# Kernel tuning notes

Hardware: AMD Instinct MI355X
Metric: run time of the kernel (lower is better)

## Reference

```python
import jax, jax.numpy as jnp
import numpy as np

N_EMBD = 384
BLOCK_SIZE = 256

def setup_inputs() -> dict:
    key = jax.random.key(0)
    k1, k2 = jax.random.split(key)
    B, T = 512, 256
    x = jax.random.normal(k1, (B, T, N_EMBD), dtype=jnp.float32)
    # nn.Linear(384, 192, bias=False): store as [in, out] so projection is x @ w
    w_qkv = jax.random.normal(k2, (N_EMBD, 3 * 64), dtype=jnp.float32) * (1.0 / np.sqrt(N_EMBD))
    return {"x": x, "w_qkv": w_qkv}

def reference(x, w_qkv):
    B, T, C = x.shape  # C == n_embd == 384
    qkv = jnp.einsum('btc,cd->btd', x, w_qkv)       # [B,T,3*hs]
    q, k, v = jnp.split(qkv, 3, axis=-1)            # each [B,T,hs]
    scale = 1.0 / jnp.sqrt(jnp.float32(C))          # NOTE: scales by full embed dim C, per source
    wei = jnp.einsum('btd,bsd->bts', q, k) * scale  # [B,T,T]
    causal = jnp.tril(jnp.ones((T, T), dtype=bool))
    wei = jnp.where(causal, wei, -jnp.inf)
    wei = jax.nn.softmax(wei, axis=-1)
    # dropout is identity in eval mode
    return jnp.einsum('bts,bsd->btd', wei, v)       # [B,T,hs]
```

## Files before the change

### kernel.cpp

```cpp
#include <hip/hip_runtime.h>
#include <hip/hip_bf16.h>


constexpr int B  = 512;
constexpr int T  = 256;
constexpr int C  = 384;
constexpr int HS = 64;
constexpr long BT = (long)B * T;
constexpr long PLANE = BT * HS;
constexpr float SCALE = 0.05103103630798288f;

constexpr int NT   = 192;
constexpr int MT   = 128;
constexpr int BK   = 64;
constexpr int ROWP = 72;
constexpr int VP   = 264;

typedef _Float16 f16x8 __attribute__((ext_vector_type(8)));
typedef _Float16 f16x4 __attribute__((ext_vector_type(4)));
typedef __fp16   fp16x2_raw __attribute__((ext_vector_type(2)));
typedef float    f32x4 __attribute__((ext_vector_type(4)));

__global__ __launch_bounds__(256)
void wt_kernel(const float* __restrict__ w, _Float16* __restrict__ wt) {
    const int idx = blockIdx.x * 256 + threadIdx.x;
    if (idx < NT * C) {
        const int n = idx / C, k = idx % C;
        wt[idx] = (_Float16)w[k * NT + n];
    }
}

__global__ __launch_bounds__(256)
void proj_kernel(const float* __restrict__ x, const _Float16* __restrict__ wt,
                 _Float16* __restrict__ qp, _Float16* __restrict__ kp,
                 _Float16* __restrict__ vtp) {
    __shared__ __align__(16) _Float16 XL[MT * ROWP];
    __shared__ __align__(16) _Float16 WL[NT * ROWP];

    const int tid  = threadIdx.x;
    const int lane = tid & 63;
    const int wv   = tid >> 6;
    const int wm   = wv >> 1, wn = wv & 1;
    const int l15  = lane & 15, quad = lane >> 4;
    const long row0 = (long)blockIdx.x * MT;

    f32x4 acc[4][6];
#pragma unroll
    for (int mi = 0; mi < 4; ++mi)
#pragma unroll
        for (int ni = 0; ni < 6; ++ni) acc[mi][ni] = (f32x4)0.f;

    for (int kc = 0; kc < C / BK; ++kc) {
        const int k0 = kc * BK;
        __syncthreads();
#pragma unroll
        for (int i = 0; i < 8; ++i) {
            const int flat = tid + 256 * i;
            const int r = flat >> 4, seg = flat & 15;
            const float4 xv = *(const float4*)(x + (row0 + r) * C + k0 + seg * 4);
            union { fp16x2_raw h[2]; uint2 u; } cvt;
            cvt.h[0] = __builtin_amdgcn_cvt_pkrtz(xv.x, xv.y);
            cvt.h[1] = __builtin_amdgcn_cvt_pkrtz(xv.z, xv.w);
            *(uint2*)&XL[r * ROWP + seg * 4] = cvt.u;
        }
#pragma unroll
        for (int i = 0; i < 6; ++i) {
            const int flat = tid + 256 * i;
            const int n = flat >> 3, seg = flat & 7;
            *(uint4*)&WL[n * ROWP + seg * 8] = *(const uint4*)(wt + n * C + k0 + seg * 8);
        }
        __syncthreads();

#pragma unroll
        for (int s = 0; s < 2; ++s) {
            const int kk = s * 32 + quad * 8;
            f16x8 a[4], bfr[6];
#pragma unroll
            for (int mi = 0; mi < 4; ++mi)
                a[mi] = *(const f16x8*)&XL[(wm * 64 + mi * 16 + l15) * ROWP + kk];
#pragma unroll
            for (int ni = 0; ni < 6; ++ni)
                bfr[ni] = *(const f16x8*)&WL[(wn * 96 + ni * 16 + l15) * ROWP + kk];
#pragma unroll
            for (int mi = 0; mi < 4; ++mi)
#pragma unroll
                for (int ni = 0; ni < 6; ++ni)
                    acc[mi][ni] = __builtin_amdgcn_mfma_f32_16x16x32_f16(
                        a[mi], bfr[ni], acc[mi][ni], 0, 0, 0);
        }
    }

#pragma unroll
    for (int mi = 0; mi < 4; ++mi) {
        const long grow0 = row0 + wm * 64 + mi * 16 + quad * 4;
        const int bb = (int)(grow0 >> 8);
        const int t0 = (int)(grow0 & 255);
#pragma unroll
        for (int ni = 0; ni < 6; ++ni) {
            const int colbase = wn * 96 + ni * 16;
            const int col = colbase + l15;
            if (colbase < 64) {
#pragma unroll
                for (int r = 0; r < 4; ++r)
                    qp[(grow0 + r) * HS + col] = (_Float16)acc[mi][ni][r];
            } else if (colbase < 128) {
#pragma unroll
                for (int r = 0; r < 4; ++r)
                    kp[(grow0 + r) * HS + (col - 64)] = (_Float16)acc[mi][ni][r];
            } else {
                f16x4 pv;
#pragma unroll
                for (int r = 0; r < 4; ++r) pv[r] = (_Float16)acc[mi][ni][r];
                *(f16x4*)&vtp[(long)bb * (HS * T) + (col - 128) * T + t0] = pv;
            }
        }
    }
}

__global__ __launch_bounds__(256)
void attn_kernel(const _Float16* __restrict__ qp, const _Float16* __restrict__ kp,
                 const _Float16* __restrict__ vtp, float* __restrict__ out) {
    __shared__ __align__(16) _Float16 VL[HS * VP];

    const int b = blockIdx.x, tid = threadIdx.x;
    const int lane = tid & 63, w = tid >> 6;
    const int l15 = lane & 15, quad = lane >> 4;

    const _Float16* Vg = vtp + (long)b * (HS * T);
#pragma unroll
    for (int i = 0; i < 8; ++i) {
        const int flat = tid + 256 * i;
        const int r = flat >> 5, seg = flat & 31;
        *(uint4*)&VL[r * VP + seg * 8] = *(const uint4*)(Vg + r * T + seg * 8);
    }
    __syncthreads();

    const _Float16* Qg = qp + ((long)b * T + w * 64) * HS;
    const _Float16* Kg = kp + (long)b * T * HS;
    f16x8 qf[4][2];
#pragma unroll
    for (int ni = 0; ni < 4; ++ni)
#pragma unroll
        for (int ks = 0; ks < 2; ++ks)
            qf[ni][ks] = *(const f16x8*)(Qg + (ni * 16 + l15) * HS + ks * 32 + quad * 8);

    f32x4 o[4][4];
#pragma unroll
    for (int di = 0; di < 4; ++di)
#pragma unroll
        for (int ni = 0; ni < 4; ++ni) o[di][ni] = (f32x4)0.f;
    float lp[4] = {0.f, 0.f, 0.f, 0.f};

    for (int c = 0; c <= w; ++c) {
        const bool diag = (c == w);
#pragma unroll
        for (int kt = 0; kt < 4; ++kt) {
            const int key0 = c * 64 + kt * 16;
            const f16x8 ka0 = *(const f16x8*)(Kg + (key0 + l15) * HS + quad * 8);
            const f16x8 ka1 = *(const f16x8*)(Kg + (key0 + l15) * HS + 32 + quad * 8);
            f16x4 va[4];
#pragma unroll
            for (int di = 0; di < 4; ++di)
                va[di] = *(const f16x4*)&VL[(di * 16 + l15) * VP + key0 + quad * 4];
#pragma unroll
            for (int ni = 0; ni < 4; ++ni) {
                if (diag && kt > ni) continue;
                f32x4 s = {0.f, 0.f, 0.f, 0.f};
                s = __builtin_amdgcn_mfma_f32_16x16x32_f16(ka0, qf[ni][0], s, 0, 0, 0);
                s = __builtin_amdgcn_mfma_f32_16x16x32_f16(ka1, qf[ni][1], s, 0, 0, 0);
                const bool dmask = diag && (kt == ni);
                f16x4 pb;
                float psum = 0.f;
#pragma unroll
                for (int r = 0; r < 4; ++r) {
                    float pr = __expf(s[r] * SCALE);
                    pr = (dmask && (quad * 4 + r > l15)) ? 0.f : pr;
                    psum += pr;
                    pb[r] = (_Float16)pr;
                }
                lp[ni] += psum;
#pragma unroll
                for (int di = 0; di < 4; ++di)
                    o[di][ni] = __builtin_amdgcn_mfma_f32_16x16x16f16(
                        va[di], pb, o[di][ni], 0, 0, 0);
            }
        }
    }

#pragma unroll
    for (int ni = 0; ni < 4; ++ni) {
        float v = lp[ni];
        v += __shfl_xor(v, 16, 64);
        v += __shfl_xor(v, 32, 64);
        lp[ni] = 1.0f / v;
    }

    float* ob = out + ((long)b * T + w * 64) * HS;
#pragma unroll
    for (int ni = 0; ni < 4; ++ni)
#pragma unroll
        for (int di = 0; di < 4; ++di) {
            float4 val;
            val.x = o[di][ni][0] * lp[ni];
            val.y = o[di][ni][1] * lp[ni];
            val.z = o[di][ni][2] * lp[ni];
            val.w = o[di][ni][3] * lp[ni];
            *(float4*)&ob[(ni * 16 + l15) * HS + di * 16 + quad * 4] = val;
        }
}

extern "C" void kernel_launch(void* const* d_in, const int* in_sizes, int n_in,
                              void* d_out, int out_size, void* d_ws, size_t ws_size,
                              hipStream_t stream) {
    const float* x = (const float*)d_in[0];
    const float* w = (const float*)d_in[1];
    float* out = (float*)d_out;

    _Float16* qp  = (_Float16*)d_ws;
    _Float16* kp  = qp + PLANE;
    _Float16* vtp = kp + PLANE;
    _Float16* wt  = vtp + PLANE;

    wt_kernel<<<dim3((NT * C + 255) / 256), dim3(256), 0, stream>>>(w, wt);
    proj_kernel<<<dim3((unsigned)(BT / MT)), dim3(256), 0, stream>>>(x, wt, qp, kp, vtp);
    attn_kernel<<<dim3(B), dim3(256), 0, stream>>>(qp, kp, vtp, out);
}
```

Before: 322.9 us.

## Fuse QKV projection and causal attention into one per-batch kernel

```diff
diff --git a/kernel.cpp b/kernel.cpp
--- a/kernel.cpp
+++ b/kernel.cpp
@@ -1,20 +1,17 @@
 #include <hip/hip_runtime.h>
-#include <hip/hip_bf16.h>
 
 
 constexpr int B  = 512;
 constexpr int T  = 256;
 constexpr int C  = 384;
 constexpr int HS = 64;
-constexpr long BT = (long)B * T;
-constexpr long PLANE = BT * HS;
-constexpr float SCALE = 0.05103103630798288f;
-
-constexpr int NT   = 192;
-constexpr int MT   = 128;
-constexpr int BK   = 64;
+constexpr int NT = 192;
+constexpr int BK = 64;
+constexpr int NKC = C / BK;
 constexpr int ROWP = 72;
 constexpr int VP   = 264;
+constexpr float SCALE = 0.05103103630798288f;
+constexpr float QSC   = SCALE * 1.4426950408889634f;
 
 typedef _Float16 f16x8 __attribute__((ext_vector_type(8)));
 typedef _Float16 f16x4 __attribute__((ext_vector_type(4)));
@@ -30,19 +27,20 @@
     }
 }
 
-__global__ __launch_bounds__(256)
-void proj_kernel(const float* __restrict__ x, const _Float16* __restrict__ wt,
-                 _Float16* __restrict__ qp, _Float16* __restrict__ kp,
-                 _Float16* __restrict__ vtp) {
-    __shared__ __align__(16) _Float16 XL[MT * ROWP];
-    __shared__ __align__(16) _Float16 WL[NT * ROWP];
+__global__ __launch_bounds__(512)
+void fused_kernel(const float* __restrict__ x, const _Float16* __restrict__ wt,
+                  float* __restrict__ out) {
+    __shared__ __align__(16) _Float16 XL[T * ROWP];
+    __shared__ __align__(16) _Float16 WL[NT * BK];
+    __shared__ __align__(16) _Float16 QL[T * HS];
+    __shared__ __align__(16) _Float16 KL[T * HS];
+    __shared__ __align__(16) _Float16 VTL[HS * VP];
 
     const int tid  = threadIdx.x;
-    const int lane = tid & 63;
-    const int wv   = tid >> 6;
+    const int lane = tid & 63, wv = tid >> 6;
+    const int l15  = lane & 15, quad = lane >> 4;
     const int wm   = wv >> 1, wn = wv & 1;
-    const int l15  = lane & 15, quad = lane >> 4;
-    const long row0 = (long)blockIdx.x * MT;
+    const float* xb = x + (long)blockIdx.x * T * C;
 
     f32x4 acc[4][6];
 #pragma unroll
@@ -50,163 +48,155 @@
 #pragma unroll
         for (int ni = 0; ni < 6; ++ni) acc[mi][ni] = (f32x4)0.f;
 
-    for (int kc = 0; kc < C / BK; ++kc) {
-        const int k0 = kc * BK;
+    float4 xv[8];
+    uint4  wvr[3];
+#pragma unroll
+    for (int i = 0; i < 8; ++i) {
+        const int flat = tid + 512 * i, r = flat >> 4, seg = flat & 15;
+        xv[i] = *(const float4*)(xb + r * C + seg * 4);
+    }
+#pragma unroll
+    for (int i = 0; i < 3; ++i) {
+        const int u = tid + 512 * i, n = u >> 3, sl = u & 7;
+        wvr[i] = *(const uint4*)(wt + n * C + sl * 8);
+    }
+
+    for (int kc = 0; kc < NKC; ++kc) {
         __syncthreads();
 #pragma unroll
         for (int i = 0; i < 8; ++i) {
-            const int flat = tid + 256 * i;
-            const int r = flat >> 4, seg = flat & 15;
-            const float4 xv = *(const float4*)(x + (row0 + r) * C + k0 + seg * 4);
-            union { fp16x2_raw h[2]; uint2 u; } cvt;
-            cvt.h[0] = __builtin_amdgcn_cvt_pkrtz(xv.x, xv.y);
-            cvt.h[1] = __builtin_amdgcn_cvt_pkrtz(xv.z, xv.w);
-            *(uint2*)&XL[r * ROWP + seg * 4] = cvt.u;
-        }
-#pragma unroll
-        for (int i = 0; i < 6; ++i) {
-            const int flat = tid + 256 * i;
-            const int n = flat >> 3, seg = flat & 7;
-            *(uint4*)&WL[n * ROWP + seg * 8] = *(const uint4*)(wt + n * C + k0 + seg * 8);
+            const int flat = tid + 512 * i, r = flat >> 4, seg = flat & 15;
+            union { fp16x2_raw h[2]; uint2 u; } cv;
+            cv.h[0] = __builtin_amdgcn_cvt_pkrtz(xv[i].x, xv[i].y);
+            cv.h[1] = __builtin_amdgcn_cvt_pkrtz(xv[i].z, xv[i].w);
+            *(uint2*)&XL[r * ROWP + seg * 4] = cv.u;
+        }
+#pragma unroll
+        for (int i = 0; i < 3; ++i) {
+            const int u = tid + 512 * i, n = u >> 3, sl = u & 7;
+            *(uint4*)&WL[n * BK + ((sl ^ (n & 7)) << 3)] = wvr[i];
         }
         __syncthreads();
-
+        if (kc + 1 < NKC) {
+            const int k0 = (kc + 1) * BK;
+#pragma unroll
+            for (int i = 0; i < 8; ++i) {
+                const int flat = tid + 512 * i, r = flat >> 4, seg = flat & 15;
+                xv[i] = *(const float4*)(xb + r * C + k0 + seg * 4);
+            }
+#pragma unroll
+            for (int i = 0; i < 3; ++i) {
+                const int u = tid + 512 * i, n = u >> 3, sl = u & 7;
+                wvr[i] = *(const uint4*)(wt + n * C + k0 + sl * 8);
+            }
+        }
 #pragma unroll
         for (int s = 0; s < 2; ++s) {
             const int kk = s * 32 + quad * 8;
-            f16x8 a[4], bfr[6];
+            const int slot = kk >> 3;
+            f16x8 a[4], bf[6];
 #pragma unroll
             for (int mi = 0; mi < 4; ++mi)
                 a[mi] = *(const f16x8*)&XL[(wm * 64 + mi * 16 + l15) * ROWP + kk];
 #pragma unroll
-            for (int ni = 0; ni < 6; ++ni)
-                bfr[ni] = *(const f16x8*)&WL[(wn * 96 + ni * 16 + l15) * ROWP + kk];
+            for (int ni = 0; ni < 6; ++ni) {
+                const int row = wn * 96 + ni * 16 + l15;
+                bf[ni] = *(const f16x8*)&WL[row * BK + ((slot ^ (row & 7)) << 3)];
+            }
 #pragma unroll
             for (int mi = 0; mi < 4; ++mi)
 #pragma unroll
                 for (int ni = 0; ni < 6; ++ni)
                     acc[mi][ni] = __builtin_amdgcn_mfma_f32_16x16x32_f16(
-                        a[mi], bfr[ni], acc[mi][ni], 0, 0, 0);
+                        a[mi], bf[ni], acc[mi][ni], 0, 0, 0);
         }
     }
 
 #pragma unroll
     for (int mi = 0; mi < 4; ++mi) {
-        const long grow0 = row0 + wm * 64 + mi * 16 + quad * 4;
-        const int bb = (int)(grow0 >> 8);
-        const int t0 = (int)(grow0 & 255);
+        const int t0 = wm * 64 + mi * 16 + quad * 4;
 #pragma unroll
         for (int ni = 0; ni < 6; ++ni) {
             const int colbase = wn * 96 + ni * 16;
             const int col = colbase + l15;
             if (colbase < 64) {
 #pragma unroll
-                for (int r = 0; r < 4; ++r)
-                    qp[(grow0 + r) * HS + col] = (_Float16)acc[mi][ni][r];
+                for (int r = 0; r < 4; ++r) {
+                    const int t = t0 + r;
+                    QL[(t * HS + col) ^ ((t & 7) << 3)] =
+                        (_Float16)(acc[mi][ni][r] * QSC);
+                }
             } else if (colbase < 128) {
 #pragma unroll
-                for (int r = 0; r < 4; ++r)
-                    kp[(grow0 + r) * HS + (col - 64)] = (_Float16)acc[mi][ni][r];
+                for (int r = 0; r < 4; ++r) {
+                    const int t = t0 + r;
+                    KL[(t * HS + (col - 64)) ^ ((t & 7) << 3)] =
+                        (_Float16)acc[mi][ni][r];
+                }
             } else {
                 f16x4 pv;
 #pragma unroll
                 for (int r = 0; r < 4; ++r) pv[r] = (_Float16)acc[mi][ni][r];
-                *(f16x4*)&vtp[(long)bb * (HS * T) + (col - 128) * T + t0] = pv;
-            }
-        }
-    }
-}
-
-__global__ __launch_bounds__(256)
-void attn_kernel(const _Float16* __restrict__ qp, const _Float16* __restrict__ kp,
-                 const _Float16* __restrict__ vtp, float* __restrict__ out) {
-    __shared__ __align__(16) _Float16 VL[HS * VP];
-
-    const int b = blockIdx.x, tid = threadIdx.x;
-    const int lane = tid & 63, w = tid >> 6;
-    const int l15 = lane & 15, quad = lane >> 4;
-
-    const _Float16* Vg = vtp + (long)b * (HS * T);
-#pragma unroll
-    for (int i = 0; i < 8; ++i) {
-        const int flat = tid + 256 * i;
-        const int r = flat >> 5, seg = flat & 31;
-        *(uint4*)&VL[r * VP + seg * 8] = *(const uint4*)(Vg + r * T + seg * 8);
+                *(f16x4*)&VTL[(col - 128) * VP + t0] = pv;
+            }
+        }
     }
     __syncthreads();
 
-    const _Float16* Qg = qp + ((long)b * T + w * 64) * HS;
-    const _Float16* Kg = kp + (long)b * T * HS;
-    f16x8 qf[4][2];
-#pragma unroll
-    for (int ni = 0; ni < 4; ++ni)
-#pragma unroll
-        for (int ks = 0; ks < 2; ++ks)
-            qf[ni][ks] = *(const f16x8*)(Qg + (ni * 16 + l15) * HS + ks * 32 + quad * 8);
-
-    f32x4 o[4][4];
-#pragma unroll
-    for (int di = 0; di < 4; ++di)
-#pragma unroll
-        for (int ni = 0; ni < 4; ++ni) o[di][ni] = (f32x4)0.f;
-    float lp[4] = {0.f, 0.f, 0.f, 0.f};
-
-    for (int c = 0; c <= w; ++c) {
-        const bool diag = (c == w);
-#pragma unroll
-        for (int kt = 0; kt < 4; ++kt) {
-            const int key0 = c * 64 + kt * 16;
-            const f16x8 ka0 = *(const f16x8*)(Kg + (key0 + l15) * HS + quad * 8);
-            const f16x8 ka1 = *(const f16x8*)(Kg + (key0 + l15) * HS + 32 + quad * 8);
+    float* ob = out + (long)blockIdx.x * T * HS;
+#pragma unroll
+    for (int pass = 0; pass < 2; ++pass) {
+        const int ch = pass ? (15 - wv) : wv;
+        const int q0 = ch * 16;
+        const int qrow = q0 + l15;
+        const f16x8 qf0 = *(const f16x8*)&QL[(qrow * HS + quad * 8) ^ ((qrow & 7) << 3)];
+        const f16x8 qf1 = *(const f16x8*)&QL[(qrow * HS + 32 + quad * 8) ^ ((qrow & 7) << 3)];
+        f32x4 o[4];
+#pragma unroll
+        for (int di = 0; di < 4; ++di) o[di] = (f32x4)0.f;
+        float lp = 0.f;
+
+        for (int kt = 0; kt <= ch; ++kt) {
+            const int k0 = kt * 16;
+            const int krow = k0 + l15;
+            const f16x8 ka0 = *(const f16x8*)&KL[(krow * HS + quad * 8) ^ ((krow & 7) << 3)];
+            const f16x8 ka1 = *(const f16x8*)&KL[(krow * HS + 32 + quad * 8) ^ ((krow & 7) << 3)];
             f16x4 va[4];
 #pragma unroll
             for (int di = 0; di < 4; ++di)
-                va[di] = *(const f16x4*)&VL[(di * 16 + l15) * VP + key0 + quad * 4];
-#pragma unroll
-            for (int ni = 0; ni < 4; ++ni) {
-                if (diag && kt > ni) continue;
-                f32x4 s = {0.f, 0.f, 0.f, 0.f};
-                s = __builtin_amdgcn_mfma_f32_16x16x32_f16(ka0, qf[ni][0], s, 0, 0, 0);
-                s = __builtin_amdgcn_mfma_f32_16x16x32_f16(ka1, qf[ni][1], s, 0, 0, 0);
-                const bool dmask = diag && (kt == ni);
-                f16x4 pb;
-                float psum = 0.f;
-#pragma unroll
-                for (int r = 0; r < 4; ++r) {
-                    float pr = __expf(s[r] * SCALE);
-                    pr = (dmask && (quad * 4 + r > l15)) ? 0.f : pr;
-                    psum += pr;
-                    pb[r] = (_Float16)pr;
-                }
-                lp[ni] += psum;
-#pragma unroll
-                for (int di = 0; di < 4; ++di)
-                    o[di][ni] = __builtin_amdgcn_mfma_f32_16x16x16f16(
-                        va[di], pb, o[di][ni], 0, 0, 0);
-            }
-        }
-    }
-
-#pragma unroll
-    for (int ni = 0; ni < 4; ++ni) {
-        float v = lp[ni];
+                va[di] = *(const f16x4*)&VTL[(di * 16 + l15) * VP + k0 + quad * 4];
+
+            f32x4 s = {0.f, 0.f, 0.f, 0.f};
+            s = __builtin_amdgcn_mfma_f32_16x16x32_f16(ka0, qf0, s, 0, 0, 0);
+            s = __builtin_amdgcn_mfma_f32_16x16x32_f16(ka1, qf1, s, 0, 0, 0);
+
+            const bool dmask = (kt == ch);
+            f16x4 pb; float psum = 0.f;
+#pragma unroll
+            for (int r = 0; r < 4; ++r) {
+                float pr = exp2f(s[r]);
+                pr = (dmask && (quad * 4 + r > l15)) ? 0.f : pr;
+                psum += pr;
+                pb[r] = (_Float16)pr;
+            }
+            lp += psum;
+#pragma unroll
+            for (int di = 0; di < 4; ++di)
+                o[di] = __builtin_amdgcn_mfma_f32_16x16x16f16(va[di], pb, o[di], 0, 0, 0);
+        }
+
+        float v = lp;
         v += __shfl_xor(v, 16, 64);
         v += __shfl_xor(v, 32, 64);
-        lp[ni] = 1.0f / v;
-    }
-
-    float* ob = out + ((long)b * T + w * 64) * HS;
-#pragma unroll
-    for (int ni = 0; ni < 4; ++ni)
+        const float inv = 1.0f / v;
 #pragma unroll
         for (int di = 0; di < 4; ++di) {
             float4 val;
-            val.x = o[di][ni][0] * lp[ni];
-            val.y = o[di][ni][1] * lp[ni];
-            val.z = o[di][ni][2] * lp[ni];
-            val.w = o[di][ni][3] * lp[ni];
-            *(float4*)&ob[(ni * 16 + l15) * HS + di * 16 + quad * 4] = val;
-        }
+            val.x = o[di][0] * inv; val.y = o[di][1] * inv;
+            val.z = o[di][2] * inv; val.w = o[di][3] * inv;
+            *(float4*)&ob[qrow * HS + di * 16 + quad * 4] = val;
+        }
+    }
 }
 
 extern "C" void kernel_launch(void* const* d_in, const int* in_sizes, int n_in,
@@ -216,12 +206,8 @@
     const float* w = (const float*)d_in[1];
     float* out = (float*)d_out;
 
-    _Float16* qp  = (_Float16*)d_ws;
-    _Float16* kp  = qp + PLANE;
-    _Float16* vtp = kp + PLANE;
-    _Float16* wt  = vtp + PLANE;
+    _Float16* wt = (_Float16*)d_ws;
 
     wt_kernel<<<dim3((NT * C + 255) / 256), dim3(256), 0, stream>>>(w, wt);
-    proj_kernel<<<dim3((unsigned)(BT / MT)), dim3(256), 0, stream>>>(x, wt, qp, kp, vtp);
-    attn_kernel<<<dim3(B), dim3(256), 0, stream>>>(qp, kp, vtp, out);
+    fused_kernel<<<dim3(B), dim3(512), 0, stream>>>(x, wt, out);
 }
```

Result: faster. 311.7 us (-3.5%).
